# Kernel optimization log

Hardware: AMD Instinct MI355X
Metric: run time of the kernel (lower is better)

The kernel has to match this reference:

```python
import jax, jax.numpy as jnp
import numpy as np

NEG = -1e9


def setup_inputs() -> dict:
    key = jax.random.key(0)
    ks = jax.random.split(key, 9)
    B, L, S, E = 8, 2048, 2048, 1024
    H, G, KD, VD = 16, 64, 1024, 1024
    return {
        "query": jax.random.normal(ks[0], (B, L, E), jnp.float32),
        "key": jax.random.normal(ks[1], (B, S, E), jnp.float32),
        "value": jax.random.normal(ks[2], (B, S, E), jnp.float32),
        "other": jnp.zeros((1,), jnp.float32),
        "key_padding_mask": jax.random.bernoulli(ks[3], 0.1, (B, S)),
        "nhead": H,
        "query_proj": jax.random.normal(ks[4], (1, E, KD), jnp.float32) * 0.02,
        "key_proj": jax.random.normal(ks[5], (1, E, KD), jnp.float32) * 0.02,
        "value_proj": jax.random.normal(ks[6], (1, E, VD), jnp.float32) * 0.02,
        "importance_proj": jax.random.normal(ks[7], (1, E, H * G), jnp.float32) * 0.02,
        "output_proj": jax.random.normal(ks[8], (1, VD, E), jnp.float32) * 0.02,
    }


def reference(query, key, value, other, key_padding_mask, nhead,
              query_proj, key_proj, value_proj, importance_proj, output_proj):
    B, L, E = query.shape
    S = key.shape[1]
    H = nhead
    KD = query_proj.shape[-1]
    VD = value_proj.shape[-1]
    Ek, Ev = KD // H, VD // H
    G = importance_proj.shape[-1] // H
    scale = 1.0 / jnp.sqrt(jnp.asarray(Ek, query.dtype))

    # projections -> (B, H, L/S, d)
    qs = (query @ query_proj[0]).reshape(B, L, H, Ek).transpose(0, 2, 1, 3)
    kk = (key @ key_proj[0]).reshape(B, S, H, Ek).transpose(0, 2, 1, 3)
    vs = (value @ value_proj[0]).reshape(B, S, H, Ev).transpose(0, 2, 1, 3)

    # importance-weighted global queries: softmax over L
    ips = (query @ importance_proj[0]).reshape(B, L, H, G).transpose(0, 2, 3, 1)  # (B,H,G,L)
    ips = jax.nn.softmax(ips, axis=-1)
    gqs = jnp.einsum('bhgl,bhld->bhgd', ips, qs)  # (B,H,G,Ek)

    # stage 1: global queries attend over all keys (shared attn for keys & values)
    g_scores = jnp.einsum('bhgd,bhsd->bhgs', gqs, kk) * scale  # (B,H,G,S)
    g_scores = jnp.where(key_padding_mask[:, None, None, :], NEG, g_scores)
    g_attn = jax.nn.softmax(g_scores, axis=-1)
    global_keys = jnp.einsum('bhgs,bhsd->bhgd', g_attn, kk)   # (B,H,G,Ek)
    global_values = jnp.einsum('bhgs,bhsd->bhgd', g_attn, vs)  # (B,H,G,Ev)

    # stage 2: local queries attend over G global keys/values
    l_scores = jnp.einsum('bhld,bhgd->bhlg', qs, global_keys) * scale  # (B,H,L,G)
    l_attn = jax.nn.softmax(l_scores, axis=-1)
    out = jnp.einsum('bhlg,bhgd->bhld', l_attn, global_values)  # (B,H,L,Ev)

    out = out.transpose(0, 2, 1, 3).reshape(B, L, H * Ev)
    out = out @ output_proj[0]  # (B,L,E)
    return (out, l_attn)
```

## Files before the change

kernel.cpp:

```cpp
#include <hip/hip_runtime.h>


typedef float f32x4 __attribute__((ext_vector_type(4)));
typedef _Float16 f16x8 __attribute__((ext_vector_type(8)));
typedef unsigned short u16;

#define DEV static __device__ __forceinline__

DEV u16 f2h(float x){
  _Float16 h = (_Float16)x;
  return __builtin_bit_cast(u16, h);
}
DEV float h2f(u16 u){
  return (float)__builtin_bit_cast(_Float16, u);
}
DEV void split1h(float x, u16 &h, u16 &l){
  h = f2h(x);
  l = f2h(x - h2f(h));
}
DEV unsigned pk2h(float a, float b){
  return (unsigned)f2h(a) | ((unsigned)f2h(b) << 16);
}

DEV void gload16(const u16* src, u16* dst_lds){
  __builtin_amdgcn_global_load_lds(
      (__attribute__((address_space(1))) void*)src,
      (__attribute__((address_space(3))) void*)dst_lds, 16, 0, 0);
}

__global__ __launch_bounds__(256)
void mask_norm(const unsigned char* __restrict__ src, unsigned char* __restrict__ dst, int n)
{
  const unsigned* w = (const unsigned*)src;
  const int tid = threadIdx.x;
  int local = 0;
  for (int i = tid; i < n/4; i += 256){
    unsigned v = w[i];
    if (v == 0x3F800000u) local |= 2;
    else if (v > 1u)      local |= 1;
  }
  __shared__ int red[256];
  red[tid] = local;
  __syncthreads();
  for (int s = 128; s; s >>= 1){
    if (tid < s) red[tid] |= red[tid+s];
    __syncthreads();
  }
  const int r = red[0];
  const int mode = (r & 2) ? 2 : ((r & 1) ? 1 : 0);
  for (int i = tid; i < n; i += 256){
    unsigned char v;
    if (mode == 1) v = src[i] ? 1 : 0;
    else           v = w[i]   ? 1 : 0;
    dst[i] = v;
  }
}

__global__ __launch_bounds__(256)
void conv_hi(const float* __restrict__ x, u16* __restrict__ hi, int n8)
{
  const int i = blockIdx.x*256 + threadIdx.x;
  if (i >= n8) return;
  f32x4 a = ((const f32x4*)x)[2*i], b = ((const f32x4*)x)[2*i+1];
  uint4 uh;
  uh.x = pk2h(a[0], a[1]); uh.y = pk2h(a[2], a[3]);
  uh.z = pk2h(b[0], b[1]); uh.w = pk2h(b[2], b[3]);
  ((uint4*)hi)[i] = uh;
}

__global__ __launch_bounds__(256)
void transpose_hi(const float* __restrict__ Wsrc, u16* __restrict__ Whi, int Kd, int Nd)
{
  __shared__ float t[64][65];
  const int tid = threadIdx.x;
  const int n0 = blockIdx.x * 64, k0 = blockIdx.y * 64;
  #pragma unroll
  for (int it = 0; it < 16; ++it){
    int e = it*256 + tid, r = e >> 6, c = e & 63;
    t[r][c] = Wsrc[(long)(k0+r)*Nd + (n0+c)];
  }
  __syncthreads();
  #pragma unroll
  for (int it = 0; it < 16; ++it){
    int e = it*256 + tid, r = e >> 6, c = e & 63;
    Whi[(long)(n0+r)*Kd + (k0+c)] = f2h(t[c][r]);
  }
}

template<int TM, int TERMS, int CM, int EPI, int SWZ>
__global__ __launch_bounds__(256)
void gemm_g(const u16* __restrict__ Ah_g, const u16* __restrict__ Al_g,
            const u16* __restrict__ Bh_g,
            void* __restrict__ Cp, void* __restrict__ Cp2,
            const unsigned char* __restrict__ maskp,
            int K, int lda, int ldb, int ldc,
            long aB, long aH, long bB, long bH, long cB, long cH,
            int H2, int Ssz, float scale)
{
  constexpr int BN = 128, BK = 32;
  constexpr int WM = TM/2, WN = BN/2;
  constexpr int FM = WM/16, FN = WN/16;
  __shared__ __align__(16) u16 AhS[2][TM*BK];
  __shared__ __align__(16) u16 AlS[2][TERMS == 2 ? TM*BK : 8];
  __shared__ __align__(16) u16 BhS[2][BN*BK];

  const int tid = threadIdx.x;
  int bx = blockIdx.x, by = blockIdx.y;
  if constexpr (SWZ){
    const int gx = gridDim.x;
    const int nwg = gx * gridDim.y;
    const int q = nwg >> 3;
    const int flat = bx + gx * by;
    const int nf = (flat & 7) * q + (flat >> 3);
    bx = nf % gx; by = nf / gx;
  }
  const int batch = blockIdx.z;
  const int b = batch / H2, h = batch - b*H2;
  const long aOff = (long)b*aB + (long)h*aH;
  const long bOff = (long)b*bB + (long)h*bH;
  const long cOff = (long)b*cB + (long)h*cH;
  const int nBase = bx * BN;
  const int mBase = by * TM;
  const int wave = tid >> 6, lane = tid & 63;
  const int wm = wave >> 1, wn = wave & 1;
  const int cg8 = (lane & 3) * 8;
  const int rsub = lane >> 2;

  auto stage = [&](int buf, int k0){
    #pragma unroll
    for (int c = 0; c < TM/64; ++c){
      const int chunk = wave*(TM/64) + c;
      const long g = aOff + (long)(mBase + chunk*16 + rsub)*lda + k0 + cg8;
      gload16(Ah_g + g, &AhS[buf][chunk*512]);
      if constexpr (TERMS == 2) gload16(Al_g + g, &AlS[buf][chunk*512]);
    }
    #pragma unroll
    for (int c = 0; c < 2; ++c){
      const int chunk = wave*2 + c;
      const long g = bOff + (long)(nBase + chunk*16 + rsub)*ldb + k0 + cg8;
      gload16(Bh_g + g, &BhS[buf][chunk*512]);
    }
  };

  f32x4 acc[FM][FN] = {};

  stage(0, 0);
  __syncthreads();
  const int nk = K >> 5;
  for (int t = 0; t < nk; ++t){
    const int buf = t & 1;
    if (t + 1 < nk) stage(buf ^ 1, (t + 1) << 5);

    f16x8 ah[FM], al[FM], bh[FN];
    #pragma unroll
    for (int mi = 0; mi < FM; ++mi){
      const int off = (wm*WM + mi*16 + (lane & 15))*BK + (lane >> 4)*8;
      ah[mi] = *(const f16x8*)&AhS[buf][off];
      if constexpr (TERMS == 2) al[mi] = *(const f16x8*)&AlS[buf][off];
    }
    #pragma unroll
    for (int ni = 0; ni < FN; ++ni){
      const int off = (wn*WN + ni*16 + (lane & 15))*BK + (lane >> 4)*8;
      bh[ni] = *(const f16x8*)&BhS[buf][off];
    }
    #pragma unroll
    for (int mi = 0; mi < FM; ++mi)
      #pragma unroll
      for (int ni = 0; ni < FN; ++ni){
        acc[mi][ni] = __builtin_amdgcn_mfma_f32_16x16x32_f16(ah[mi], bh[ni], acc[mi][ni], 0, 0, 0);
        if constexpr (TERMS == 2)
          acc[mi][ni] = __builtin_amdgcn_mfma_f32_16x16x32_f16(al[mi], bh[ni], acc[mi][ni], 0, 0, 0);
      }
    __syncthreads();
  }

  const int cr = (lane >> 4) * 4, cc = lane & 15;
  #pragma unroll
  for (int mi = 0; mi < FM; ++mi)
    #pragma unroll
    for (int ni = 0; ni < FN; ++ni)
      #pragma unroll
      for (int r = 0; r < 4; ++r){
        const int row = mBase + wm*WM + mi*16 + cr + r;
        const int col = nBase + wn*WN + ni*16 + cc;
        float v = acc[mi][ni][r];
        if constexpr (EPI == 1){
          v *= scale;
          if (maskp[(long)b*Ssz + col]) v = -1e9f;
        }
        const long ci = cOff + (long)row*ldc + col;
        if constexpr (CM == 0){
          ((float*)Cp)[ci] = v;
        } else {
          u16 hh, ll;
          split1h(v, hh, ll);
          ((u16*)Cp)[ci]  = hh;
          ((u16*)Cp2)[ci] = ll;
        }
      }
}

__global__ __launch_bounds__(256)
void softmax_inplace(float* __restrict__ data, int Wd)
{
  float* rp = data + (long)blockIdx.x * Wd;
  const int tid = threadIdx.x;
  const int lane = tid & 63, wv = tid >> 6;
  f32x4 v0 = ((const f32x4*)rp)[tid*2];
  f32x4 v1 = ((const f32x4*)rp)[tid*2+1];
  float m = fmaxf(fmaxf(fmaxf(v0[0],v0[1]),fmaxf(v0[2],v0[3])),
                  fmaxf(fmaxf(v1[0],v1[1]),fmaxf(v1[2],v1[3])));
  #pragma unroll
  for (int off = 32; off; off >>= 1) m = fmaxf(m, __shfl_xor(m, off));
  __shared__ float rm[4], rs[4];
  if (lane == 0) rm[wv] = m;
  __syncthreads();
  m = fmaxf(fmaxf(rm[0],rm[1]), fmaxf(rm[2],rm[3]));
  f32x4 e0, e1;
  #pragma unroll
  for (int i = 0; i < 4; ++i){ e0[i] = __expf(v0[i]-m); e1[i] = __expf(v1[i]-m); }
  float s = (e0[0]+e0[1]+e0[2]+e0[3]) + (e1[0]+e1[1]+e1[2]+e1[3]);
  #pragma unroll
  for (int off = 32; off; off >>= 1) s += __shfl_xor(s, off);
  if (lane == 0) rs[wv] = s;
  __syncthreads();
  s = (rs[0]+rs[1]) + (rs[2]+rs[3]);
  const float inv = 1.0f / s;
  ((f32x4*)rp)[tid*2]   = e0 * inv;
  ((f32x4*)rp)[tid*2+1] = e1 * inv;
}

__global__ __launch_bounds__(256)
void einsum64(const float* __restrict__ A,
              const u16* __restrict__ Bhip, const u16* __restrict__ Blop,
              float* __restrict__ Cpart,
              int K, int KC, int lda, int ldb,
              long aB, long aH, long bB, long bH, int H2, int nbatch)
{
  __shared__ float As[64][68];
  __shared__ float Bs[64][68];
  const int tid = threadIdx.x;
  const int kc = blockIdx.x, batch = blockIdx.y;
  const int b = batch / H2, h = batch - b*H2;
  const float* Ab = A + (long)b*aB + (long)h*aH;
  const u16* Bh = Bhip + (long)b*bB + (long)h*bH;
  const u16* Bl = Blop + (long)b*bB + (long)h*bH;
  const int kchunk = K / KC, kbeg = kc * kchunk;
  const int tm = tid >> 4, tn = tid & 15;
  const int sr = tid >> 4, sc = (tid & 15) * 4;
  float acc[4][4] = {};
  for (int ks = kbeg; ks < kbeg + kchunk; ks += 64){
    if (ks != kbeg) __syncthreads();
    #pragma unroll
    for (int p = 0; p < 4; ++p){
      const int g = p*16 + sr;
      f32x4 av = *(const f32x4*)&Ab[(long)g*lda + ks + sc];
      As[sc+0][g] = av[0]; As[sc+1][g] = av[1];
      As[sc+2][g] = av[2]; As[sc+3][g] = av[3];
      const int kr = p*16 + sr;
      ushort4 h4 = *(const ushort4*)&Bh[(long)(ks+kr)*ldb + sc];
      ushort4 l4 = *(const ushort4*)&Bl[(long)(ks+kr)*ldb + sc];
      Bs[kr][sc+0] = h2f(h4.x) + h2f(l4.x);
      Bs[kr][sc+1] = h2f(h4.y) + h2f(l4.y);
      Bs[kr][sc+2] = h2f(h4.z) + h2f(l4.z);
      Bs[kr][sc+3] = h2f(h4.w) + h2f(l4.w);
    }
    __syncthreads();
    #pragma unroll 8
    for (int k = 0; k < 64; ++k){
      f32x4 a4 = *(const f32x4*)&As[k][tm*4];
      f32x4 b4 = *(const f32x4*)&Bs[k][tn*4];
      #pragma unroll
      for (int i = 0; i < 4; ++i)
        #pragma unroll
        for (int j = 0; j < 4; ++j)
          acc[i][j] += a4[i] * b4[j];
    }
  }
  float* outp = Cpart + ((long)(kc*nbatch + batch) << 12);
  #pragma unroll
  for (int i = 0; i < 4; ++i){
    f32x4 v = { acc[i][0], acc[i][1], acc[i][2], acc[i][3] };
    *(f32x4*)&outp[(tm*4+i)*64 + tn*4] = v;
  }
}

__global__ __launch_bounds__(256)
void einsum64_dual(const float* __restrict__ A,
                   const u16* __restrict__ B1h, const u16* __restrict__ B1l,
                   const u16* __restrict__ B2h, const u16* __restrict__ B2l,
                   float* __restrict__ P1, float* __restrict__ P2,
                   int K, int KC, int lda, int ldb,
                   long aB, long aH, long bB, long bH, int H2, int nbatch)
{
  __shared__ float As[64][68];
  __shared__ float B1s[64][68];
  __shared__ float B2s[64][68];
  const int tid = threadIdx.x;
  const int kc = blockIdx.x, batch = blockIdx.y;
  const int b = batch / H2, h = batch - b*H2;
  const float* Ab = A + (long)b*aB + (long)h*aH;
  const u16* b1h = B1h + (long)b*bB + (long)h*bH;
  const u16* b1l = B1l + (long)b*bB + (long)h*bH;
  const u16* b2h = B2h + (long)b*bB + (long)h*bH;
  const u16* b2l = B2l + (long)b*bB + (long)h*bH;
  const int kchunk = K / KC, kbeg = kc * kchunk;
  const int tm = tid >> 4, tn = tid & 15;
  const int sr = tid >> 4, sc = (tid & 15) * 4;
  float acc1[4][4] = {}, acc2[4][4] = {};
  for (int ks = kbeg; ks < kbeg + kchunk; ks += 64){
    if (ks != kbeg) __syncthreads();
    #pragma unroll
    for (int p = 0; p < 4; ++p){
      const int g = p*16 + sr;
      f32x4 av = *(const f32x4*)&Ab[(long)g*lda + ks + sc];
      As[sc+0][g] = av[0]; As[sc+1][g] = av[1];
      As[sc+2][g] = av[2]; As[sc+3][g] = av[3];
      const int kr = p*16 + sr;
      ushort4 h4 = *(const ushort4*)&b1h[(long)(ks+kr)*ldb + sc];
      ushort4 l4 = *(const ushort4*)&b1l[(long)(ks+kr)*ldb + sc];
      B1s[kr][sc+0] = h2f(h4.x) + h2f(l4.x);
      B1s[kr][sc+1] = h2f(h4.y) + h2f(l4.y);
      B1s[kr][sc+2] = h2f(h4.z) + h2f(l4.z);
      B1s[kr][sc+3] = h2f(h4.w) + h2f(l4.w);
      h4 = *(const ushort4*)&b2h[(long)(ks+kr)*ldb + sc];
      l4 = *(const ushort4*)&b2l[(long)(ks+kr)*ldb + sc];
      B2s[kr][sc+0] = h2f(h4.x) + h2f(l4.x);
      B2s[kr][sc+1] = h2f(h4.y) + h2f(l4.y);
      B2s[kr][sc+2] = h2f(h4.z) + h2f(l4.z);
      B2s[kr][sc+3] = h2f(h4.w) + h2f(l4.w);
    }
    __syncthreads();
    #pragma unroll 4
    for (int k = 0; k < 64; ++k){
      f32x4 a4 = *(const f32x4*)&As[k][tm*4];
      f32x4 b4 = *(const f32x4*)&B1s[k][tn*4];
      f32x4 c4 = *(const f32x4*)&B2s[k][tn*4];
      #pragma unroll
      for (int i = 0; i < 4; ++i)
        #pragma unroll
        for (int j = 0; j < 4; ++j){
          acc1[i][j] += a4[i] * b4[j];
          acc2[i][j] += a4[i] * c4[j];
        }
    }
  }
  const long po = ((long)(kc*nbatch + batch) << 12);
  #pragma unroll
  for (int i = 0; i < 4; ++i){
    f32x4 v1 = { acc1[i][0], acc1[i][1], acc1[i][2], acc1[i][3] };
    f32x4 v2 = { acc2[i][0], acc2[i][1], acc2[i][2], acc2[i][3] };
    *(f32x4*)&P1[po + (tm*4+i)*64 + tn*4] = v1;
    *(f32x4*)&P2[po + (tm*4+i)*64 + tn*4] = v2;
  }
}

__global__ __launch_bounds__(256)
void reduce64(const float* __restrict__ part,
              u16* __restrict__ outhi, u16* __restrict__ outlo,
              int n4, int parts)
{
  const int idx = blockIdx.x*256 + threadIdx.x;
  if (idx >= n4) return;
  f32x4 s = ((const f32x4*)part)[idx];
  for (int p = 1; p < parts; ++p) s += ((const f32x4*)part)[(long)p*n4 + idx];
  ushort4 uh, ul;
  split1h(s[0], uh.x, ul.x); split1h(s[1], uh.y, ul.y);
  split1h(s[2], uh.z, ul.z); split1h(s[3], uh.w, ul.w);
  ((ushort4*)outhi)[idx] = uh;
  ((ushort4*)outlo)[idx] = ul;
}

__global__ __launch_bounds__(256)
void stage2_mfma(const u16* __restrict__ qhi, const u16* __restrict__ qlo,
                 const u16* __restrict__ gkh_g, const u16* __restrict__ gkl_g,
                 const u16* __restrict__ gvh_g, const u16* __restrict__ gvl_g,
                 float* __restrict__ lattn, u16* __restrict__ ahi,
                 float scale)
{
  __shared__ __align__(16) u16 Ah[128][72];
  __shared__ __align__(16) u16 Al[128][72];
  __shared__ __align__(16) u16 Bh[64][72];
  __shared__ __align__(16) u16 Bl[64][72];
  const int tid = threadIdx.x;
  const int bh = blockIdx.y;
  const int b = bh >> 4, h = bh & 15;
  const int l0 = blockIdx.x * 128;
  const int wm = tid >> 6, lane = tid & 63;

  const long qbase = ((long)b*2048 + l0)*1024 + h*64;
  #pragma unroll
  for (int it = 0; it < 4; ++it){
    const int e = it*256 + tid, row = e >> 3, s = e & 7;
    const long g = qbase + (long)row*1024 + s*8;
    *(uint4*)&Ah[row][s*8] = *(const uint4*)(qhi + g);
    *(uint4*)&Al[row][s*8] = *(const uint4*)(qlo + g);
  }
  const long gb = (long)bh * 4096;
  #pragma unroll
  for (int it = 0; it < 2; ++it){
    const int e = it*256 + tid, gr = e >> 3, s = e & 7;
    *(uint4*)&Bh[gr][s*8] = *(const uint4*)(gkh_g + gb + gr*64 + s*8);
    *(uint4*)&Bl[gr][s*8] = *(const uint4*)(gkl_g + gb + gr*64 + s*8);
  }
  __syncthreads();

  f32x4 acc[2][4] = {};
  #pragma unroll
  for (int k0 = 0; k0 < 64; k0 += 32){
    f16x8 a_h[2], a_l[2], b_h[4], b_l[4];
    #pragma unroll
    for (int mi = 0; mi < 2; ++mi){
      const int row = wm*32 + mi*16 + (lane & 15);
      a_h[mi] = *(const f16x8*)&Ah[row][k0 + (lane >> 4)*8];
      a_l[mi] = *(const f16x8*)&Al[row][k0 + (lane >> 4)*8];
    }
    #pragma unroll
    for (int ni = 0; ni < 4; ++ni){
      const int nr = ni*16 + (lane & 15);
      b_h[ni] = *(const f16x8*)&Bh[nr][k0 + (lane >> 4)*8];
      b_l[ni] = *(const f16x8*)&Bl[nr][k0 + (lane >> 4)*8];
    }
    #pragma unroll
    for (int mi = 0; mi < 2; ++mi)
      #pragma unroll
      for (int ni = 0; ni < 4; ++ni){
        acc[mi][ni] = __builtin_amdgcn_mfma_f32_16x16x32_f16(a_h[mi], b_h[ni], acc[mi][ni], 0, 0, 0);
        acc[mi][ni] = __builtin_amdgcn_mfma_f32_16x16x32_f16(a_l[mi], b_h[ni], acc[mi][ni], 0, 0, 0);
        acc[mi][ni] = __builtin_amdgcn_mfma_f32_16x16x32_f16(a_h[mi], b_l[ni], acc[mi][ni], 0, 0, 0);
      }
  }
  __syncthreads();

  #pragma unroll
  for (int it = 0; it < 4; ++it){
    const int e = it*256 + tid;
    const int gr = e >> 4, d0 = (e & 15) * 4;
    ushort4 vh = *(const ushort4*)(gvh_g + gb + gr*64 + d0);
    ushort4 vl = *(const ushort4*)(gvl_g + gb + gr*64 + d0);
    Bh[d0+0][gr] = vh.x; Bh[d0+1][gr] = vh.y; Bh[d0+2][gr] = vh.z; Bh[d0+3][gr] = vh.w;
    Bl[d0+0][gr] = vl.x; Bl[d0+1][gr] = vl.y; Bl[d0+2][gr] = vl.z; Bl[d0+3][gr] = vl.w;
  }

  #pragma unroll
  for (int mi = 0; mi < 2; ++mi){
    #pragma unroll
    for (int r = 0; r < 4; ++r){
      float v0 = acc[mi][0][r]*scale, v1 = acc[mi][1][r]*scale;
      float v2 = acc[mi][2][r]*scale, v3 = acc[mi][3][r]*scale;
      float mx = fmaxf(fmaxf(v0,v1), fmaxf(v2,v3));
      #pragma unroll
      for (int off = 1; off < 16; off <<= 1) mx = fmaxf(mx, __shfl_xor(mx, off, 16));
      float e0 = __expf(v0-mx), e1 = __expf(v1-mx), e2 = __expf(v2-mx), e3 = __expf(v3-mx);
      float sum = (e0+e1) + (e2+e3);
      #pragma unroll
      for (int off = 1; off < 16; off <<= 1) sum += __shfl_xor(sum, off, 16);
      const float inv = 1.0f / sum;
      e0 *= inv; e1 *= inv; e2 *= inv; e3 *= inv;
      const int lrow = wm*32 + mi*16 + (lane >> 4)*4 + r;
      float* lp = lattn + ((long)bh*2048 + l0 + lrow)*64 + (lane & 15);
      lp[0] = e0; lp[16] = e1; lp[32] = e2; lp[48] = e3;
      u16 hh, ll;
      split1h(e0, hh, ll); Ah[lrow][ 0 + (lane&15)] = hh; Al[lrow][ 0 + (lane&15)] = ll;
      split1h(e1, hh, ll); Ah[lrow][16 + (lane&15)] = hh; Al[lrow][16 + (lane&15)] = ll;
      split1h(e2, hh, ll); Ah[lrow][32 + (lane&15)] = hh; Al[lrow][32 + (lane&15)] = ll;
      split1h(e3, hh, ll); Ah[lrow][48 + (lane&15)] = hh; Al[lrow][48 + (lane&15)] = ll;
    }
  }
  __syncthreads();

  f32x4 o[2][4] = {};
  #pragma unroll
  for (int k0 = 0; k0 < 64; k0 += 32){
    f16x8 p_h[2], p_l[2], b_h[4], b_l[4];
    #pragma unroll
    for (int mi = 0; mi < 2; ++mi){
      const int row = wm*32 + mi*16 + (lane & 15);
      p_h[mi] = *(const f16x8*)&Ah[row][k0 + (lane >> 4)*8];
      p_l[mi] = *(const f16x8*)&Al[row][k0 + (lane >> 4)*8];
    }
    #pragma unroll
    for (int ni = 0; ni < 4; ++ni){
      const int nr = ni*16 + (lane & 15);
      b_h[ni] = *(const f16x8*)&Bh[nr][k0 + (lane >> 4)*8];
      b_l[ni] = *(const f16x8*)&Bl[nr][k0 + (lane >> 4)*8];
    }
    #pragma unroll
    for (int mi = 0; mi < 2; ++mi)
      #pragma unroll
      for (int ni = 0; ni < 4; ++ni){
        o[mi][ni] = __builtin_amdgcn_mfma_f32_16x16x32_f16(p_h[mi], b_h[ni], o[mi][ni], 0, 0, 0);
        o[mi][ni] = __builtin_amdgcn_mfma_f32_16x16x32_f16(p_l[mi], b_h[ni], o[mi][ni], 0, 0, 0);
        o[mi][ni] = __builtin_amdgcn_mfma_f32_16x16x32_f16(p_h[mi], b_l[ni], o[mi][ni], 0, 0, 0);
      }
  }

  #pragma unroll
  for (int mi = 0; mi < 2; ++mi)
    #pragma unroll
    for (int ni = 0; ni < 4; ++ni)
      #pragma unroll
      for (int r = 0; r < 4; ++r){
        const int lrow = wm*32 + mi*16 + (lane >> 4)*4 + r;
        const int d = ni*16 + (lane & 15);
        const long oidx = ((long)b*2048 + l0 + lrow)*1024 + h*64 + d;
        ahi[oidx] = f2h(o[mi][ni][r]);
      }
}

extern "C" void kernel_launch(void* const* d_in, const int* in_sizes, int n_in,
                              void* d_out, int out_size, void* d_ws, size_t ws_size,
                              hipStream_t stream)
{
  const float* query = (const float*)d_in[0];
  const float* key   = (const float*)d_in[1];
  const float* value = (const float*)d_in[2];
  const unsigned char* mask_raw = (const unsigned char*)d_in[4];
  const float* Wq = (const float*)d_in[6];
  const float* Wk = (const float*)d_in[7];
  const float* Wv = (const float*)d_in[8];
  const float* Wi = (const float*)d_in[9];
  const float* Wo = (const float*)d_in[10];
  float* out0 = (float*)d_out;
  float* out1 = out0 + 16777216;

  char* ws = (char*)d_ws;
  u16* WoT_hi = (u16*)(ws + 0);
  u16* WqT_hi = (u16*)(ws + (4L<<20));
  u16* WkT_hi = (u16*)(ws + (8L<<20));
  u16* WvT_hi = (u16*)(ws + (12L<<20));
  u16* WiT_hi = (u16*)(ws + (16L<<20));
  u16* qp_hi = (u16*)(ws + (20L<<20));
  u16* kp_hi = qp_hi;
  u16* vp_hi = qp_hi;
  float* gsc  = (float*)(ws + (20L<<20));
  u16* qs_hi  = (u16*)(ws + (84L<<20));
  u16* qs_lo  = (u16*)(ws + (116L<<20));
  u16* vs_hi  = (u16*)(ws + (148L<<20));
  u16* vs_lo  = (u16*)(ws + (180L<<20));
  float* ips  = (float*)(ws + (212L<<20));
  u16* kk_hi  = (u16*)(ws + (212L<<20));
  u16* kk_lo  = (u16*)(ws + (244L<<20));
  u16* attn_hi = kk_hi;
  float* part1 = (float*)(ws + (4L<<20));
  float* part2 = (float*)(ws + (12L<<20));
  u16* gk_hi = (u16*)(ws + (10L<<20));
  u16* gk_lo = (u16*)(ws + (11L<<20));
  u16* gv_hi = (u16*)(ws + (14L<<20));
  u16* gv_lo = (u16*)(ws + (15L<<20));
  unsigned char* mask_ws = (unsigned char*)(ws + (18L<<20));
  u16* gqs_hi = (u16*)(ws + (17L<<20));
  u16* gqs_lo = (u16*)(ws + (19L<<20));
  gv_hi = (u16*)(ws + (2L<<20));
  gv_lo = (u16*)(ws + (3L<<20));

  const dim3 blk(256);
  const float scale = 0.125f;

  transpose_hi<<<dim3(16,16), blk, 0, stream>>>(Wq, WqT_hi, 1024, 1024);
  transpose_hi<<<dim3(16,16), blk, 0, stream>>>(Wk, WkT_hi, 1024, 1024);
  transpose_hi<<<dim3(16,16), blk, 0, stream>>>(Wv, WvT_hi, 1024, 1024);
  transpose_hi<<<dim3(16,16), blk, 0, stream>>>(Wi, WiT_hi, 1024, 1024);
  transpose_hi<<<dim3(16,16), blk, 0, stream>>>(Wo, WoT_hi, 1024, 1024);

  conv_hi<<<8192, blk, 0, stream>>>(query, qp_hi, 2097152);

  gemm_g<128,1,1,0,1><<<dim3(8,128,1), blk, 0, stream>>>(
      qp_hi, nullptr, WqT_hi, qs_hi, qs_lo, nullptr,
      1024, 1024,1024,1024, 0,0, 0,0, 0,0, 1, 2048, 1.f);

  gemm_g<128,1,0,0,0><<<dim3(16,8,8), blk, 0, stream>>>(
      WiT_hi, nullptr, qp_hi, ips, nullptr, nullptr,
      1024, 1024,1024,2048, 0,0, 2097152L,0, 2097152L,0, 1, 2048, 1.f);
  mask_norm<<<1, blk, 0, stream>>>(mask_raw, mask_ws, 16384);
  softmax_inplace<<<8192, blk, 0, stream>>>(ips, 2048);

  einsum64<<<dim3(2,128), blk, 0, stream>>>(ips, qs_hi, qs_lo, part1,
      2048, 2, 2048, 1024, 2097152L, 131072L, 2097152L, 64L, 16, 128);
  reduce64<<<512, blk, 0, stream>>>(part1, gqs_hi, gqs_lo, 131072, 2);

  conv_hi<<<8192, blk, 0, stream>>>(key, kp_hi, 2097152);
  gemm_g<128,1,1,0,1><<<dim3(8,128,1), blk, 0, stream>>>(
      kp_hi, nullptr, WkT_hi, kk_hi, kk_lo, nullptr,
      1024, 1024,1024,1024, 0,0, 0,0, 0,0, 1, 2048, 1.f);

  conv_hi<<<8192, blk, 0, stream>>>(value, vp_hi, 2097152);
  gemm_g<128,1,1,0,1><<<dim3(8,128,1), blk, 0, stream>>>(
      vp_hi, nullptr, WvT_hi, vs_hi, vs_lo, nullptr,
      1024, 1024,1024,1024, 0,0, 0,0, 0,0, 1, 2048, 1.f);

  gemm_g<64,2,0,1,0><<<dim3(16,1,128), blk, 0, stream>>>(
      gqs_hi, gqs_lo, kk_hi, gsc, nullptr, mask_ws,
      64, 64,1024,2048, 65536L,4096L, 2097152L,64L, 2097152L,131072L, 16, 2048, scale);
  softmax_inplace<<<8192, blk, 0, stream>>>(gsc, 2048);

  einsum64_dual<<<dim3(2,128), blk, 0, stream>>>(gsc, kk_hi, kk_lo, vs_hi, vs_lo,
      part1, part2, 2048, 2, 2048, 1024, 2097152L, 131072L, 2097152L, 64L, 16, 128);
  reduce64<<<512, blk, 0, stream>>>(part1, gk_hi, gk_lo, 131072, 2);
  reduce64<<<512, blk, 0, stream>>>(part2, gv_hi, gv_lo, 131072, 2);

  stage2_mfma<<<dim3(16,128), blk, 0, stream>>>(qs_hi, qs_lo, gk_hi, gk_lo,
      gv_hi, gv_lo, out1, attn_hi, scale);

  gemm_g<128,1,0,0,1><<<dim3(8,128,1), blk, 0, stream>>>(
      attn_hi, nullptr, WoT_hi, out0, nullptr, nullptr,
      1024, 1024,1024,1024, 0,0, 0,0, 0,0, 1, 2048, 1.f);

  (void)in_sizes; (void)n_in; (void)out_size; (void)ws_size;
}
```

Baseline: 624.5 us.

## Move importance and global-attention einsums to split-fp16 MFMA with split softmax storage

Replaces the scalar FP32 einsum64/einsum64_dual kernels with a templated MFMA kernel that does 3-term split-fp16 products (hi*hi, lo*hi, hi*lo). The score GEMMs now write hi/lo fp16 pairs, and a new softmax kernel reads and writes that split format, which halves score-buffer traffic. K-split goes from 2 to 4 for more parallelism. The workspace layout is reshuffled to match, and the mask fill value changes to -50000 so it fits in fp16. Dropping the lo*lo term and using fp16 storage may cost some precision.

```diff
diff --git a/kernel.cpp b/kernel.cpp
--- a/kernel.cpp
+++ b/kernel.cpp
@@ -186,7 +186,7 @@
         float v = acc[mi][ni][r];
         if constexpr (EPI == 1){
           v *= scale;
-          if (maskp[(long)b*Ssz + col]) v = -1e9f;
+          if (maskp[(long)b*Ssz + col]) v = -50000.0f;
         }
         const long ci = cOff + (long)row*ldc + col;
         if constexpr (CM == 0){
@@ -201,158 +201,141 @@
 }
 
 __global__ __launch_bounds__(256)
-void softmax_inplace(float* __restrict__ data, int Wd)
-{
-  float* rp = data + (long)blockIdx.x * Wd;
+void softmax_split(u16* __restrict__ hi, u16* __restrict__ lo)
+{
+  const long base = (long)blockIdx.x * 2048;
   const int tid = threadIdx.x;
   const int lane = tid & 63, wv = tid >> 6;
-  f32x4 v0 = ((const f32x4*)rp)[tid*2];
-  f32x4 v1 = ((const f32x4*)rp)[tid*2+1];
-  float m = fmaxf(fmaxf(fmaxf(v0[0],v0[1]),fmaxf(v0[2],v0[3])),
-                  fmaxf(fmaxf(v1[0],v1[1]),fmaxf(v1[2],v1[3])));
+  uint4 uh = ((const uint4*)(hi + base))[tid];
+  uint4 ul = ((const uint4*)(lo + base))[tid];
+  float v[8];
+  v[0] = h2f((u16)uh.x) + h2f((u16)ul.x);
+  v[1] = h2f((u16)(uh.x>>16)) + h2f((u16)(ul.x>>16));
+  v[2] = h2f((u16)uh.y) + h2f((u16)ul.y);
+  v[3] = h2f((u16)(uh.y>>16)) + h2f((u16)(ul.y>>16));
+  v[4] = h2f((u16)uh.z) + h2f((u16)ul.z);
+  v[5] = h2f((u16)(uh.z>>16)) + h2f((u16)(ul.z>>16));
+  v[6] = h2f((u16)uh.w) + h2f((u16)ul.w);
+  v[7] = h2f((u16)(uh.w>>16)) + h2f((u16)(ul.w>>16));
+  float m = v[0];
+  #pragma unroll
+  for (int i = 1; i < 8; ++i) m = fmaxf(m, v[i]);
   #pragma unroll
   for (int off = 32; off; off >>= 1) m = fmaxf(m, __shfl_xor(m, off));
   __shared__ float rm[4], rs[4];
   if (lane == 0) rm[wv] = m;
   __syncthreads();
   m = fmaxf(fmaxf(rm[0],rm[1]), fmaxf(rm[2],rm[3]));
-  f32x4 e0, e1;
-  #pragma unroll
-  for (int i = 0; i < 4; ++i){ e0[i] = __expf(v0[i]-m); e1[i] = __expf(v1[i]-m); }
-  float s = (e0[0]+e0[1]+e0[2]+e0[3]) + (e1[0]+e1[1]+e1[2]+e1[3]);
+  float s = 0.f;
+  #pragma unroll
+  for (int i = 0; i < 8; ++i){ v[i] = __expf(v[i]-m); s += v[i]; }
   #pragma unroll
   for (int off = 32; off; off >>= 1) s += __shfl_xor(s, off);
   if (lane == 0) rs[wv] = s;
   __syncthreads();
   s = (rs[0]+rs[1]) + (rs[2]+rs[3]);
   const float inv = 1.0f / s;
-  ((f32x4*)rp)[tid*2]   = e0 * inv;
-  ((f32x4*)rp)[tid*2+1] = e1 * inv;
-}
-
-__global__ __launch_bounds__(256)
-void einsum64(const float* __restrict__ A,
-              const u16* __restrict__ Bhip, const u16* __restrict__ Blop,
-              float* __restrict__ Cpart,
+  u16 hh[8], ll[8];
+  #pragma unroll
+  for (int i = 0; i < 8; ++i) split1h(v[i]*inv, hh[i], ll[i]);
+  uh.x = (unsigned)hh[0] | ((unsigned)hh[1]<<16);
+  uh.y = (unsigned)hh[2] | ((unsigned)hh[3]<<16);
+  uh.z = (unsigned)hh[4] | ((unsigned)hh[5]<<16);
+  uh.w = (unsigned)hh[6] | ((unsigned)hh[7]<<16);
+  ul.x = (unsigned)ll[0] | ((unsigned)ll[1]<<16);
+  ul.y = (unsigned)ll[2] | ((unsigned)ll[3]<<16);
+  ul.z = (unsigned)ll[4] | ((unsigned)ll[5]<<16);
+  ul.w = (unsigned)ll[6] | ((unsigned)ll[7]<<16);
+  ((uint4*)(hi + base))[tid] = uh;
+  ((uint4*)(lo + base))[tid] = ul;
+}
+
+template<int NB>
+__global__ __launch_bounds__(256)
+void einsum_m(const u16* __restrict__ Ah_g, const u16* __restrict__ Al_g,
+              const u16* __restrict__ B1h_g, const u16* __restrict__ B1l_g,
+              const u16* __restrict__ B2h_g, const u16* __restrict__ B2l_g,
+              float* __restrict__ P1, float* __restrict__ P2,
               int K, int KC, int lda, int ldb,
               long aB, long aH, long bB, long bH, int H2, int nbatch)
 {
-  __shared__ float As[64][68];
-  __shared__ float Bs[64][68];
+  __shared__ __align__(16) u16 AhS[64][72];
+  __shared__ __align__(16) u16 AlS[64][72];
+  __shared__ __align__(16) u16 B1hS[64][72];
+  __shared__ __align__(16) u16 B1lS[64][72];
+  __shared__ __align__(16) u16 B2hS[NB==2?64:1][72];
+  __shared__ __align__(16) u16 B2lS[NB==2?64:1][72];
   const int tid = threadIdx.x;
   const int kc = blockIdx.x, batch = blockIdx.y;
   const int b = batch / H2, h = batch - b*H2;
-  const float* Ab = A + (long)b*aB + (long)h*aH;
-  const u16* Bh = Bhip + (long)b*bB + (long)h*bH;
-  const u16* Bl = Blop + (long)b*bB + (long)h*bH;
+  const long aOff = (long)b*aB + (long)h*aH;
+  const long bOff = (long)b*bB + (long)h*bH;
   const int kchunk = K / KC, kbeg = kc * kchunk;
-  const int tm = tid >> 4, tn = tid & 15;
-  const int sr = tid >> 4, sc = (tid & 15) * 4;
-  float acc[4][4] = {};
+  const int wm = tid >> 6, lane = tid & 63;
+  const int ar = tid >> 3, as = (tid & 7) * 8;
+
+  f32x4 acc1[4] = {};
+  f32x4 acc2[4] = {};
+
   for (int ks = kbeg; ks < kbeg + kchunk; ks += 64){
     if (ks != kbeg) __syncthreads();
     #pragma unroll
-    for (int p = 0; p < 4; ++p){
-      const int g = p*16 + sr;
-      f32x4 av = *(const f32x4*)&Ab[(long)g*lda + ks + sc];
-      As[sc+0][g] = av[0]; As[sc+1][g] = av[1];
-      As[sc+2][g] = av[2]; As[sc+3][g] = av[3];
-      const int kr = p*16 + sr;
-      ushort4 h4 = *(const ushort4*)&Bh[(long)(ks+kr)*ldb + sc];
-      ushort4 l4 = *(const ushort4*)&Bl[(long)(ks+kr)*ldb + sc];
-      Bs[kr][sc+0] = h2f(h4.x) + h2f(l4.x);
-      Bs[kr][sc+1] = h2f(h4.y) + h2f(l4.y);
-      Bs[kr][sc+2] = h2f(h4.z) + h2f(l4.z);
-      Bs[kr][sc+3] = h2f(h4.w) + h2f(l4.w);
+    for (int it = 0; it < 2; ++it){
+      const int g = it*32 + ar;
+      const long ga = aOff + (long)g*lda + ks + as;
+      *(uint4*)&AhS[g][as] = *(const uint4*)(Ah_g + ga);
+      *(uint4*)&AlS[g][as] = *(const uint4*)(Al_g + ga);
+    }
+    #pragma unroll
+    for (int it = 0; it < 4; ++it){
+      const int e = it*256 + tid;
+      const int lr = e >> 4, d0 = (e & 15) * 4;
+      const long gm = bOff + (long)(ks + lr)*ldb + d0;
+      ushort4 h4 = *(const ushort4*)(B1h_g + gm);
+      ushort4 l4 = *(const ushort4*)(B1l_g + gm);
+      B1hS[d0+0][lr]=h4.x; B1hS[d0+1][lr]=h4.y; B1hS[d0+2][lr]=h4.z; B1hS[d0+3][lr]=h4.w;
+      B1lS[d0+0][lr]=l4.x; B1lS[d0+1][lr]=l4.y; B1lS[d0+2][lr]=l4.z; B1lS[d0+3][lr]=l4.w;
+      if constexpr (NB == 2){
+        ushort4 h42 = *(const ushort4*)(B2h_g + gm);
+        ushort4 l42 = *(const ushort4*)(B2l_g + gm);
+        B2hS[d0+0][lr]=h42.x; B2hS[d0+1][lr]=h42.y; B2hS[d0+2][lr]=h42.z; B2hS[d0+3][lr]=h42.w;
+        B2lS[d0+0][lr]=l42.x; B2lS[d0+1][lr]=l42.y; B2lS[d0+2][lr]=l42.z; B2lS[d0+3][lr]=l42.w;
+      }
     }
     __syncthreads();
-    #pragma unroll 8
-    for (int k = 0; k < 64; ++k){
-      f32x4 a4 = *(const f32x4*)&As[k][tm*4];
-      f32x4 b4 = *(const f32x4*)&Bs[k][tn*4];
-      #pragma unroll
-      for (int i = 0; i < 4; ++i)
-        #pragma unroll
-        for (int j = 0; j < 4; ++j)
-          acc[i][j] += a4[i] * b4[j];
-    }
-  }
-  float* outp = Cpart + ((long)(kc*nbatch + batch) << 12);
-  #pragma unroll
-  for (int i = 0; i < 4; ++i){
-    f32x4 v = { acc[i][0], acc[i][1], acc[i][2], acc[i][3] };
-    *(f32x4*)&outp[(tm*4+i)*64 + tn*4] = v;
-  }
-}
-
-__global__ __launch_bounds__(256)
-void einsum64_dual(const float* __restrict__ A,
-                   const u16* __restrict__ B1h, const u16* __restrict__ B1l,
-                   const u16* __restrict__ B2h, const u16* __restrict__ B2l,
-                   float* __restrict__ P1, float* __restrict__ P2,
-                   int K, int KC, int lda, int ldb,
-                   long aB, long aH, long bB, long bH, int H2, int nbatch)
-{
-  __shared__ float As[64][68];
-  __shared__ float B1s[64][68];
-  __shared__ float B2s[64][68];
-  const int tid = threadIdx.x;
-  const int kc = blockIdx.x, batch = blockIdx.y;
-  const int b = batch / H2, h = batch - b*H2;
-  const float* Ab = A + (long)b*aB + (long)h*aH;
-  const u16* b1h = B1h + (long)b*bB + (long)h*bH;
-  const u16* b1l = B1l + (long)b*bB + (long)h*bH;
-  const u16* b2h = B2h + (long)b*bB + (long)h*bH;
-  const u16* b2l = B2l + (long)b*bB + (long)h*bH;
-  const int kchunk = K / KC, kbeg = kc * kchunk;
-  const int tm = tid >> 4, tn = tid & 15;
-  const int sr = tid >> 4, sc = (tid & 15) * 4;
-  float acc1[4][4] = {}, acc2[4][4] = {};
-  for (int ks = kbeg; ks < kbeg + kchunk; ks += 64){
-    if (ks != kbeg) __syncthreads();
-    #pragma unroll
-    for (int p = 0; p < 4; ++p){
-      const int g = p*16 + sr;
-      f32x4 av = *(const f32x4*)&Ab[(long)g*lda + ks + sc];
-      As[sc+0][g] = av[0]; As[sc+1][g] = av[1];
-      As[sc+2][g] = av[2]; As[sc+3][g] = av[3];
-      const int kr = p*16 + sr;
-      ushort4 h4 = *(const ushort4*)&b1h[(long)(ks+kr)*ldb + sc];
-      ushort4 l4 = *(const ushort4*)&b1l[(long)(ks+kr)*ldb + sc];
-      B1s[kr][sc+0] = h2f(h4.x) + h2f(l4.x);
-      B1s[kr][sc+1] = h2f(h4.y) + h2f(l4.y);
-      B1s[kr][sc+2] = h2f(h4.z) + h2f(l4.z);
-      B1s[kr][sc+3] = h2f(h4.w) + h2f(l4.w);
-      h4 = *(const ushort4*)&b2h[(long)(ks+kr)*ldb + sc];
-      l4 = *(const ushort4*)&b2l[(long)(ks+kr)*ldb + sc];
-      B2s[kr][sc+0] = h2f(h4.x) + h2f(l4.x);
-      B2s[kr][sc+1] = h2f(h4.y) + h2f(l4.y);
-      B2s[kr][sc+2] = h2f(h4.z) + h2f(l4.z);
-      B2s[kr][sc+3] = h2f(h4.w) + h2f(l4.w);
-    }
-    __syncthreads();
-    #pragma unroll 4
-    for (int k = 0; k < 64; ++k){
-      f32x4 a4 = *(const f32x4*)&As[k][tm*4];
-      f32x4 b4 = *(const f32x4*)&B1s[k][tn*4];
-      f32x4 c4 = *(const f32x4*)&B2s[k][tn*4];
-      #pragma unroll
-      for (int i = 0; i < 4; ++i)
-        #pragma unroll
-        for (int j = 0; j < 4; ++j){
-          acc1[i][j] += a4[i] * b4[j];
-          acc2[i][j] += a4[i] * c4[j];
+    #pragma unroll
+    for (int k0 = 0; k0 < 64; k0 += 32){
+      const int ko = k0 + (lane >> 4)*8;
+      const int fr = lane & 15;
+      f16x8 a_h = *(const f16x8*)&AhS[wm*16 + fr][ko];
+      f16x8 a_l = *(const f16x8*)&AlS[wm*16 + fr][ko];
+      #pragma unroll
+      for (int ni = 0; ni < 4; ++ni){
+        f16x8 b_h = *(const f16x8*)&B1hS[ni*16 + fr][ko];
+        f16x8 b_l = *(const f16x8*)&B1lS[ni*16 + fr][ko];
+        acc1[ni] = __builtin_amdgcn_mfma_f32_16x16x32_f16(a_h, b_h, acc1[ni], 0, 0, 0);
+        acc1[ni] = __builtin_amdgcn_mfma_f32_16x16x32_f16(a_l, b_h, acc1[ni], 0, 0, 0);
+        acc1[ni] = __builtin_amdgcn_mfma_f32_16x16x32_f16(a_h, b_l, acc1[ni], 0, 0, 0);
+        if constexpr (NB == 2){
+          f16x8 c_h = *(const f16x8*)&B2hS[ni*16 + fr][ko];
+          f16x8 c_l = *(const f16x8*)&B2lS[ni*16 + fr][ko];
+          acc2[ni] = __builtin_amdgcn_mfma_f32_16x16x32_f16(a_h, c_h, acc2[ni], 0, 0, 0);
+          acc2[ni] = __builtin_amdgcn_mfma_f32_16x16x32_f16(a_l, c_h, acc2[ni], 0, 0, 0);
+          acc2[ni] = __builtin_amdgcn_mfma_f32_16x16x32_f16(a_h, c_l, acc2[ni], 0, 0, 0);
         }
+      }
     }
   }
   const long po = ((long)(kc*nbatch + batch) << 12);
-  #pragma unroll
-  for (int i = 0; i < 4; ++i){
-    f32x4 v1 = { acc1[i][0], acc1[i][1], acc1[i][2], acc1[i][3] };
-    f32x4 v2 = { acc2[i][0], acc2[i][1], acc2[i][2], acc2[i][3] };
-    *(f32x4*)&P1[po + (tm*4+i)*64 + tn*4] = v1;
-    *(f32x4*)&P2[po + (tm*4+i)*64 + tn*4] = v2;
-  }
+  const int cr = (lane >> 4) * 4, cc = lane & 15;
+  #pragma unroll
+  for (int ni = 0; ni < 4; ++ni)
+    #pragma unroll
+    for (int r = 0; r < 4; ++r){
+      const int g = wm*16 + cr + r, d = ni*16 + cc;
+      P1[po + g*64 + d] = acc1[ni][r];
+      if constexpr (NB == 2) P2[po + g*64 + d] = acc2[ni][r];
+    }
 }
 
 __global__ __launch_bounds__(256)
@@ -529,30 +512,31 @@
   u16* WqT_hi = (u16*)(ws + (4L<<20));
   u16* WkT_hi = (u16*)(ws + (8L<<20));
   u16* WvT_hi = (u16*)(ws + (12L<<20));
-  u16* WiT_hi = (u16*)(ws + (16L<<20));
+  u16* WiT_hi = (u16*)(ws + (18L<<20));
+  unsigned char* mask_ws = (unsigned char*)(ws + (6L<<20));
+  u16* gqs_hi = (u16*)(ws + (16L<<20));
+  u16* gqs_lo = (u16*)(ws + (17L<<20));
+  float* part1 = (float*)(ws + (4L<<20));
+  float* part2 = (float*)(ws + (12L<<20));
   u16* qp_hi = (u16*)(ws + (20L<<20));
   u16* kp_hi = qp_hi;
   u16* vp_hi = qp_hi;
-  float* gsc  = (float*)(ws + (20L<<20));
+  u16* gsc_hi = (u16*)(ws + (20L<<20));
+  u16* gsc_lo = (u16*)(ws + (52L<<20));
   u16* qs_hi  = (u16*)(ws + (84L<<20));
   u16* qs_lo  = (u16*)(ws + (116L<<20));
+  float* partg = (float*)(ws + (148L<<20));
   u16* vs_hi  = (u16*)(ws + (148L<<20));
   u16* vs_lo  = (u16*)(ws + (180L<<20));
-  float* ips  = (float*)(ws + (212L<<20));
+  u16* ips_hi = (u16*)(ws + (212L<<20));
+  u16* ips_lo = (u16*)(ws + (244L<<20));
   u16* kk_hi  = (u16*)(ws + (212L<<20));
   u16* kk_lo  = (u16*)(ws + (244L<<20));
-  u16* attn_hi = kk_hi;
-  float* part1 = (float*)(ws + (4L<<20));
-  float* part2 = (float*)(ws + (12L<<20));
-  u16* gk_hi = (u16*)(ws + (10L<<20));
-  u16* gk_lo = (u16*)(ws + (11L<<20));
-  u16* gv_hi = (u16*)(ws + (14L<<20));
-  u16* gv_lo = (u16*)(ws + (15L<<20));
-  unsigned char* mask_ws = (unsigned char*)(ws + (18L<<20));
-  u16* gqs_hi = (u16*)(ws + (17L<<20));
-  u16* gqs_lo = (u16*)(ws + (19L<<20));
-  gv_hi = (u16*)(ws + (2L<<20));
-  gv_lo = (u16*)(ws + (3L<<20));
+  u16* gk_hi  = (u16*)(ws + (212L<<20));
+  u16* gk_lo  = (u16*)(ws + (213L<<20));
+  u16* gv_hi  = (u16*)(ws + (214L<<20));
+  u16* gv_lo  = (u16*)(ws + (215L<<20));
+  u16* attn_hi = (u16*)(ws + (244L<<20));
 
   const dim3 blk(256);
   const float scale = 0.125f;
@@ -569,15 +553,16 @@
       qp_hi, nullptr, WqT_hi, qs_hi, qs_lo, nullptr,
       1024, 1024,1024,1024, 0,0, 0,0, 0,0, 1, 2048, 1.f);
 
-  gemm_g<128,1,0,0,0><<<dim3(16,8,8), blk, 0, stream>>>(
-      WiT_hi, nullptr, qp_hi, ips, nullptr, nullptr,
+  gemm_g<128,1,1,0,0><<<dim3(16,8,8), blk, 0, stream>>>(
+      WiT_hi, nullptr, qp_hi, ips_hi, ips_lo, nullptr,
       1024, 1024,1024,2048, 0,0, 2097152L,0, 2097152L,0, 1, 2048, 1.f);
   mask_norm<<<1, blk, 0, stream>>>(mask_raw, mask_ws, 16384);
-  softmax_inplace<<<8192, blk, 0, stream>>>(ips, 2048);
-
-  einsum64<<<dim3(2,128), blk, 0, stream>>>(ips, qs_hi, qs_lo, part1,
-      2048, 2, 2048, 1024, 2097152L, 131072L, 2097152L, 64L, 16, 128);
-  reduce64<<<512, blk, 0, stream>>>(part1, gqs_hi, gqs_lo, 131072, 2);
+  softmax_split<<<8192, blk, 0, stream>>>(ips_hi, ips_lo);
+
+  einsum_m<1><<<dim3(4,128), blk, 0, stream>>>(
+      ips_hi, ips_lo, qs_hi, qs_lo, nullptr, nullptr, partg, nullptr,
+      2048, 4, 2048, 1024, 2097152L, 131072L, 2097152L, 64L, 16, 128);
+  reduce64<<<512, blk, 0, stream>>>(partg, gqs_hi, gqs_lo, 131072, 4);
 
   conv_hi<<<8192, blk, 0, stream>>>(key, kp_hi, 2097152);
   gemm_g<128,1,1,0,1><<<dim3(8,128,1), blk, 0, stream>>>(
@@ -589,15 +574,16 @@
       vp_hi, nullptr, WvT_hi, vs_hi, vs_lo, nullptr,
       1024, 1024,1024,1024, 0,0, 0,0, 0,0, 1, 2048, 1.f);
 
-  gemm_g<64,2,0,1,0><<<dim3(16,1,128), blk, 0, stream>>>(
-      gqs_hi, gqs_lo, kk_hi, gsc, nullptr, mask_ws,
+  gemm_g<64,2,1,1,0><<<dim3(16,1,128), blk, 0, stream>>>(
+      gqs_hi, gqs_lo, kk_hi, gsc_hi, gsc_lo, mask_ws,
       64, 64,1024,2048, 65536L,4096L, 2097152L,64L, 2097152L,131072L, 16, 2048, scale);
-  softmax_inplace<<<8192, blk, 0, stream>>>(gsc, 2048);
-
-  einsum64_dual<<<dim3(2,128), blk, 0, stream>>>(gsc, kk_hi, kk_lo, vs_hi, vs_lo,
-      part1, part2, 2048, 2, 2048, 1024, 2097152L, 131072L, 2097152L, 64L, 16, 128);
-  reduce64<<<512, blk, 0, stream>>>(part1, gk_hi, gk_lo, 131072, 2);
-  reduce64<<<512, blk, 0, stream>>>(part2, gv_hi, gv_lo, 131072, 2);
+  softmax_split<<<8192, blk, 0, stream>>>(gsc_hi, gsc_lo);
+
+  einsum_m<2><<<dim3(4,128), blk, 0, stream>>>(
+      gsc_hi, gsc_lo, kk_hi, kk_lo, vs_hi, vs_lo, part1, part2,
+      2048, 4, 2048, 1024, 2097152L, 131072L, 2097152L, 64L, 16, 128);
+  reduce64<<<512, blk, 0, stream>>>(part1, gk_hi, gk_lo, 131072, 4);
+  reduce64<<<512, blk, 0, stream>>>(part2, gv_hi, gv_lo, 131072, 4);
 
   stage2_mfma<<<dim3(16,128), blk, 0, stream>>>(qs_hi, qs_lo, gk_hi, gk_lo,
       gv_hi, gv_lo, out1, attn_hi, scale);
```

After: 576.5 us. 7.7% less time.
